# Performance work log

Hardware: AMD Instinct MI355X
Metric: run time of the kernel (lower is better)

Reference implementation:

```python
import jax, jax.numpy as jnp
import numpy as np

B, T, V, D = 8, 256, 32, 256


def setup_inputs() -> dict:
    key = jax.random.key(0)
    k1, k2 = jax.random.split(key)
    # scale by 0.1 so exp(q.k) stays well within fp32 range (dot std ~ 0.1^2*sqrt(D))
    feature = jax.random.normal(k1, (B, T, V, D), dtype=jnp.float32) * 0.1
    feature_aug = jax.random.normal(k2, (B, T, V, D), dtype=jnp.float32) * 0.1
    return {"feature": feature, "feature_aug": feature_aug}


def reference(feature, feature_aug):
    # match torch permute(0,2,1,3): [B,T,V,D] -> [B,V,T,D]
    f = jnp.transpose(feature, (0, 2, 1, 3))      # [B,V,Tq,D]
    fa = jnp.transpose(feature_aug, (0, 2, 1, 3))  # [B,V,Tk,D]
    # all-pairs QK^T scores: [B_i, B_j, V, Tq, Tk]
    scores = jnp.einsum('ivqd,jvkd->ijvqk', f, fa)
    E = jnp.exp(scores)
    # positive (j == i): ap = exp(scores[i,i]).sum over V, Tq -> [B, Tk]
    diag = jnp.einsum('iivqk->ivqk', E)           # [B,V,Tq,Tk]
    ap_exp = diag.sum(axis=(1, 2))                # [B, Tk]
    # negatives (j != i): sum over j,V,Tk minus the j==i part -> [B, Tq]
    total = E.sum(axis=(1, 2, 4))                 # [B, Tq]
    self_part = diag.sum(axis=(1, 3))             # [B, Tq]
    an_exp = total - self_part                    # [B, Tq]
    # per-anchor loss vector [T]; original sums over anchors then takes .mean()
    loss_vec = -jnp.log(ap_exp / an_exp)          # [B, T]
    return loss_vec.sum(axis=0).mean()
```

## Files before the change

kernel.cpp:

```cpp
#include <hip/hip_runtime.h>
#include <hip/hip_bf16.h>


typedef __attribute__((ext_vector_type(4))) float f32x4;
typedef __attribute__((ext_vector_type(2))) long long i64x2;
typedef __attribute__((ext_vector_type(8))) __bf16 bf16x8;
typedef long long i64;

#if __has_builtin(__builtin_amdgcn_exp2f)
#define EXP2(x) __builtin_amdgcn_exp2f(x)
#else
#define EXP2(x) exp2f(x)
#endif

__device__ __forceinline__ unsigned short f2bf(float f) {
    unsigned u = __builtin_bit_cast(unsigned, f);
    u += 0x7FFFu + ((u >> 16) & 1u);
    return (unsigned short)(u >> 16);
}

template <bool HI>
__device__ __forceinline__ unsigned cvt2fp8(float a, float b, unsigned old) {
    return __builtin_amdgcn_cvt_pk_fp8_f32(a, b, old, HI);
}
__device__ __forceinline__ unsigned pack4fp8(float x, float y, float z, float w) {
    return cvt2fp8<true>(z, w, cvt2fp8<false>(x, y, 0u));
}

__device__ __forceinline__ void async16(const void* g, void* l) {
    __builtin_amdgcn_global_load_lds(
        (const __attribute__((address_space(1))) unsigned int*)g,
        (__attribute__((address_space(3))) unsigned int*)l,
        16, 0, 0);
}

template <int CTRL>
__device__ __forceinline__ float dpp_add(float x) {
    int y = __builtin_amdgcn_update_dpp(0, __builtin_bit_cast(int, x),
                                        CTRL, 0xf, 0xf, true);
    return x + __builtin_bit_cast(float, y);
}
__device__ __forceinline__ float rowsum16(float x) {
    x = dpp_add<0x111>(x);
    x = dpp_add<0x112>(x);
    x = dpp_add<0x114>(x);
    x = dpp_add<0x118>(x);
    return x;
}

__global__ __launch_bounds__(256) void infonce_repack_fp8(
    const float* __restrict__ feat, const float* __restrict__ feat_aug,
    unsigned char* __restrict__ pA, unsigned char* __restrict__ pB,
    float* __restrict__ counters)
{
    const int row = blockIdx.x;
    const int tid = threadIdx.x;
    if (blockIdx.x == 0 && blockIdx.y == 0) {
        #pragma unroll
        for (int k = 0; k < 24; ++k) counters[k * 256 + tid] = 0.f;
    }
    const bool isA = (blockIdx.y == 0);
    const float sc = isA ? 1.4426950408889634f : 1.0f;
    const float* src = (isA ? feat : feat_aug) + (size_t)row * 8192;
    unsigned char* dst = (isA ? pA : pB) + (size_t)row * 8192;
    #pragma unroll
    for (int it = 0; it < 2; ++it) {
        const int ob = it * 4096 + tid * 16;
        const int v = ob >> 8;
        const int s = (ob >> 6) & 3;
        const int g = (ob >> 4) & 3;
        const int f1 = v * 256 + s * 64 + g * 8;
        const int f2 = f1 + 32;
        const float4 a0 = *(const float4*)(src + f1);
        const float4 a1 = *(const float4*)(src + f1 + 4);
        const float4 b0 = *(const float4*)(src + f2);
        const float4 b1 = *(const float4*)(src + f2 + 4);
        uint4 p;
        p.x = pack4fp8(a0.x*sc, a0.y*sc, a0.z*sc, a0.w*sc);
        p.y = pack4fp8(a1.x*sc, a1.y*sc, a1.z*sc, a1.w*sc);
        p.z = pack4fp8(b0.x*sc, b0.y*sc, b0.z*sc, b0.w*sc);
        p.w = pack4fp8(b1.x*sc, b1.y*sc, b1.z*sc, b1.w*sc);
        *(uint4*)(dst + ob) = p;
    }
}

__global__ __launch_bounds__(256) void infonce_main_fp8(
    const unsigned char* __restrict__ pA, const unsigned char* __restrict__ pB,
    float* __restrict__ total, float* __restrict__ selfp, float* __restrict__ ap)
{
    __shared__ __align__(16) unsigned char As[2][8192];
    __shared__ __align__(16) unsigned char Bs[2][8192];
    __shared__ float ls_row2[2][128];
    __shared__ float ls_col2[2][128];

    const int tid  = threadIdx.x;
    const int lane = tid & 63;
    const int w    = tid >> 6;
    const int wm   = w >> 1;
    const int wn   = w & 1;
    const int lrow = lane & 15;
    const int quad = lane >> 4;

    const int tileM = blockIdx.x & 15;
    const int tileN = blockIdx.x >> 4;
    const int v     = blockIdx.y;
    const bool diag = (tileM >> 1) == (tileN >> 1);

    const int rl  = w * 32 + (lane >> 2);
    const int cgg = (lane & 3) ^ ((lane >> 3) & 3);
    const unsigned char* aG = pA + ((size_t)(tileM*128 + rl) * 32 + v) * 256 + cgg * 16;
    const unsigned char* bG = pB + ((size_t)(tileN*128 + rl) * 32 + v) * 256 + cgg * 16;

    f32x4 acc[4][4];
    #pragma unroll
    for (int i = 0; i < 4; ++i)
        #pragma unroll
        for (int j = 0; j < 4; ++j)
            acc[i][j] = (f32x4){0.f, 0.f, 0.f, 0.f};

    #pragma unroll
    for (int i = 0; i < 2; ++i) {
        async16(aG + (size_t)i * 16 * 8192, &As[0][w * 2048 + i * 1024]);
        async16(bG + (size_t)i * 16 * 8192, &Bs[0][w * 2048 + i * 1024]);
    }
    __syncthreads();

    const int cgp = (quad ^ ((lrow >> 1) & 3)) * 16;

    #pragma unroll
    for (int s = 0; s < 4; ++s) {
        const int b = s & 1;
        if (s < 3) {
            const int nb = b ^ 1;
            #pragma unroll
            for (int i = 0; i < 2; ++i) {
                async16(aG + (size_t)i * 16 * 8192 + (s + 1) * 64,
                        &As[nb][w * 2048 + i * 1024]);
                async16(bG + (size_t)i * 16 * 8192 + (s + 1) * 64,
                        &Bs[nb][w * 2048 + i * 1024]);
            }
        }
        i64x2 a4[4], b4[4];
        #pragma unroll
        for (int t = 0; t < 4; ++t) {
            a4[t] = *(const i64x2*)&As[b][(wm * 64 + t * 16 + lrow) * 64 + cgp];
            b4[t] = *(const i64x2*)&Bs[b][(wn * 64 + t * 16 + lrow) * 64 + cgp];
        }
        #pragma unroll
        for (int kh = 0; kh < 2; ++kh)
            #pragma unroll
            for (int ti = 0; ti < 4; ++ti)
                #pragma unroll
                for (int tj = 0; tj < 4; ++tj)
                    acc[ti][tj] = __builtin_amdgcn_mfma_f32_16x16x32_fp8_fp8(
                        a4[ti][kh], b4[tj][kh], acc[ti][tj], 0, 0, 0);
        __syncthreads();
    }

    float colp[4] = {0.f, 0.f, 0.f, 0.f};
    #pragma unroll
    for (int ti = 0; ti < 4; ++ti) {
        #pragma unroll
        for (int r = 0; r < 4; ++r) {
            float e0 = EXP2(acc[ti][0][r]);
            float e1 = EXP2(acc[ti][1][r]);
            float e2 = EXP2(acc[ti][2][r]);
            float e3 = EXP2(acc[ti][3][r]);
            if (diag) { colp[0] += e0; colp[1] += e1; colp[2] += e2; colp[3] += e3; }
            float rp = rowsum16((e0 + e1) + (e2 + e3));
            if (lrow == 15)
                ls_row2[wn][wm * 64 + ti * 16 + quad * 4 + r] = rp;
        }
    }
    if (diag) {
        #pragma unroll
        for (int tj = 0; tj < 4; ++tj) {
            float q = colp[tj];
            q += __shfl_xor(q, 16);
            q += __shfl_xor(q, 32);
            if (lane < 16)
                ls_col2[wm][wn * 64 + tj * 16 + lane] = q;
        }
    }
    __syncthreads();
    if (tid < 128) {
        const float rs = ls_row2[0][tid] + ls_row2[1][tid];
        const int rowg = tileM * 128 + tid;
        atomicAdd(&total[rowg], rs);
        if (diag) atomicAdd(&selfp[rowg], rs);
    } else if (diag) {
        const int t2 = tid - 128;
        atomicAdd(&ap[tileN * 128 + t2], ls_col2[0][t2] + ls_col2[1][t2]);
    }
}

__global__ __launch_bounds__(256) void infonce_main_slow(
    const float* __restrict__ feat, const float* __restrict__ feat_aug,
    float* __restrict__ total, float* __restrict__ selfp, float* __restrict__ ap)
{
    __shared__ __align__(16) unsigned short As[128][72];
    __shared__ __align__(16) unsigned short Bs[128][72];
    __shared__ float ls_row[128];
    __shared__ float ls_col[128];

    const int tid  = threadIdx.x;
    const int lane = tid & 63;
    const int w    = tid >> 6;
    const int wm   = w >> 1;
    const int wn   = w & 1;
    const int lrow = lane & 15;
    const int quad = lane >> 4;

    const int tileM = blockIdx.x & 15;
    const int tileN = blockIdx.x >> 4;
    const int v     = blockIdx.y;
    const bool diag = (tileM >> 1) == (tileN >> 1);

    if (tid < 128) ls_row[tid] = 0.0f;
    else           ls_col[tid - 128] = 0.0f;

    const float* aBase = feat     + (size_t)v * 256;
    const float* bBase = feat_aug + (size_t)v * 256;

    f32x4 acc[4][4];
    #pragma unroll
    for (int i = 0; i < 4; ++i)
        #pragma unroll
        for (int j = 0; j < 4; ++j)
            acc[i][j] = (f32x4){0.f, 0.f, 0.f, 0.f};

    const int srow = tid >> 4;
    const int scol = (tid & 15) * 4;

    for (int s = 0; s < 4; ++s) {
        const int k0 = s * 64;
        if (s) __syncthreads();
        #pragma unroll
        for (int it = 0; it < 8; ++it) {
            const int row = it * 16 + srow;
            const float4 a4 = *(const float4*)(aBase + (size_t)(tileM * 128 + row) * 8192 + k0 + scol);
            const float4 b4 = *(const float4*)(bBase + (size_t)(tileN * 128 + row) * 8192 + k0 + scol);
            uint2 wa, wb;
            wa.x = (unsigned)f2bf(a4.x) | ((unsigned)f2bf(a4.y) << 16);
            wa.y = (unsigned)f2bf(a4.z) | ((unsigned)f2bf(a4.w) << 16);
            wb.x = (unsigned)f2bf(b4.x) | ((unsigned)f2bf(b4.y) << 16);
            wb.y = (unsigned)f2bf(b4.z) | ((unsigned)f2bf(b4.w) << 16);
            *(uint2*)&As[row][scol] = wa;
            *(uint2*)&Bs[row][scol] = wb;
        }
        __syncthreads();
        #pragma unroll
        for (int kk = 0; kk < 64; kk += 32) {
            bf16x8 af[4], bfr[4];
            #pragma unroll
            for (int t = 0; t < 4; ++t) {
                af[t]  = *(const bf16x8*)&As[wm * 64 + t * 16 + lrow][kk + quad * 8];
                bfr[t] = *(const bf16x8*)&Bs[wn * 64 + t * 16 + lrow][kk + quad * 8];
            }
            #pragma unroll
            for (int ti = 0; ti < 4; ++ti)
                #pragma unroll
                for (int tj = 0; tj < 4; ++tj)
                    acc[ti][tj] = __builtin_amdgcn_mfma_f32_16x16x32_bf16(
                        af[ti], bfr[tj], acc[ti][tj], 0, 0, 0);
        }
    }

    float colp[4] = {0.f, 0.f, 0.f, 0.f};
    #pragma unroll
    for (int ti = 0; ti < 4; ++ti) {
        #pragma unroll
        for (int r = 0; r < 4; ++r) {
            float e0 = __expf(acc[ti][0][r]);
            float e1 = __expf(acc[ti][1][r]);
            float e2 = __expf(acc[ti][2][r]);
            float e3 = __expf(acc[ti][3][r]);
            colp[0] += e0; colp[1] += e1; colp[2] += e2; colp[3] += e3;
            float rp = (e0 + e1) + (e2 + e3);
            rp += __shfl_xor(rp, 1);
            rp += __shfl_xor(rp, 2);
            rp += __shfl_xor(rp, 4);
            rp += __shfl_xor(rp, 8);
            if (lrow == 0)
                atomicAdd(&ls_row[wm * 64 + ti * 16 + quad * 4 + r], rp);
        }
    }
    if (diag) {
        #pragma unroll
        for (int tj = 0; tj < 4; ++tj) {
            float q = colp[tj];
            q += __shfl_xor(q, 16);
            q += __shfl_xor(q, 32);
            if (lane < 16)
                atomicAdd(&ls_col[wn * 64 + tj * 16 + lane], q);
        }
    }
    __syncthreads();
    if (tid < 128) {
        const float rs = ls_row[tid];
        const int rowg = tileM * 128 + tid;
        atomicAdd(&total[rowg], rs);
        if (diag) atomicAdd(&selfp[rowg], rs);
    } else if (diag) {
        const int t2 = tid - 128;
        atomicAdd(&ap[tileN * 128 + t2], ls_col[t2]);
    }
}

__global__ __launch_bounds__(256) void infonce_finalize(
    const float* __restrict__ total, const float* __restrict__ selfp,
    const float* __restrict__ ap, float* __restrict__ out)
{
    __shared__ float red[4];
    const int tid = threadIdx.x;
    float s = 0.f;
    for (int e = tid; e < 2048; e += 256) {
        const float an = total[e] - selfp[e];
        s += logf(an / ap[e]);
    }
    #pragma unroll
    for (int m = 32; m >= 1; m >>= 1) s += __shfl_xor(s, m);
    if ((tid & 63) == 0) red[tid >> 6] = s;
    __syncthreads();
    if (tid == 0) out[0] = (red[0] + red[1] + red[2] + red[3]) * (1.0f / 256.0f);
}

extern "C" void kernel_launch(void* const* d_in, const int* in_sizes, int n_in,
                              void* d_out, int out_size, void* d_ws, size_t ws_size,
                              hipStream_t stream) {
    const float* feat     = (const float*)d_in[0];
    const float* feat_aug = (const float*)d_in[1];
    float* total = (float*)d_ws;
    float* selfp = total + 2048;
    float* ap    = selfp + 2048;

    const size_t packBytes = (size_t)2048 * 8192;
    const size_t need = 32768 + 2 * packBytes;
    if (ws_size >= need) {
        unsigned char* pA = (unsigned char*)d_ws + 32768;
        unsigned char* pB = pA + packBytes;
        infonce_repack_fp8<<<dim3(2048, 2), 256, 0, stream>>>(feat, feat_aug, pA, pB, total);
        infonce_main_fp8<<<dim3(256, 32), 256, 0, stream>>>(pA, pB, total, selfp, ap);
    } else {
        (void)hipMemsetAsync(d_ws, 0, 3 * 2048 * sizeof(float), stream);
        infonce_main_slow<<<dim3(256, 32), 256, 0, stream>>>(feat, feat_aug, total, selfp, ap);
    }
    infonce_finalize<<<1, 256, 0, stream>>>(total, selfp, ap, (float*)d_out);
}
```

Measured before the change: 207.6 us.

## Switch main GEMM to scaled 16x16x128 MFMA with full-K LDS tile

Replaces the 16x16x32 fp8 MFMA chain with the gfx950 scaled mfma_scale_f32_16x16x128_f8f6f4 (unit scales), cutting the number of MFMA issues per tile by four. The whole K=256 slice for A and B is now loaded into LDS in one shot with an XOR swizzle, instead of a 4-stage double-buffered pipeline, and the repack kernel becomes a plain contiguous conversion. The row/col partial buffers alias the A tile in LDS. The larger 64KB LDS footprint with launch_bounds(256,2) may limit occupancy, and the load/compute overlap from the old pipeline is gone.

```diff
diff --git a/kernel.cpp b/kernel.cpp
--- a/kernel.cpp
+++ b/kernel.cpp
@@ -3,9 +3,9 @@
 
 
 typedef __attribute__((ext_vector_type(4))) float f32x4;
-typedef __attribute__((ext_vector_type(2))) long long i64x2;
+typedef __attribute__((ext_vector_type(4))) int   i32x4;
+typedef __attribute__((ext_vector_type(8))) int   i32x8;
 typedef __attribute__((ext_vector_type(8))) __bf16 bf16x8;
-typedef long long i64;
 
 #if __has_builtin(__builtin_amdgcn_exp2f)
 #define EXP2(x) __builtin_amdgcn_exp2f(x)
@@ -32,6 +32,13 @@
         (const __attribute__((address_space(1))) unsigned int*)g,
         (__attribute__((address_space(3))) unsigned int*)l,
         16, 0, 0);
+}
+
+__device__ __forceinline__ i32x8 cat8(i32x4 lo, i32x4 hi) {
+    i32x8 r;
+    r[0] = lo[0]; r[1] = lo[1]; r[2] = lo[2]; r[3] = lo[3];
+    r[4] = hi[0]; r[5] = hi[1]; r[6] = hi[2]; r[7] = hi[3];
+    return r;
 }
 
 template <int CTRL>
@@ -65,33 +72,28 @@
     unsigned char* dst = (isA ? pA : pB) + (size_t)row * 8192;
     #pragma unroll
     for (int it = 0; it < 2; ++it) {
-        const int ob = it * 4096 + tid * 16;
-        const int v = ob >> 8;
-        const int s = (ob >> 6) & 3;
-        const int g = (ob >> 4) & 3;
-        const int f1 = v * 256 + s * 64 + g * 8;
-        const int f2 = f1 + 32;
-        const float4 a0 = *(const float4*)(src + f1);
-        const float4 a1 = *(const float4*)(src + f1 + 4);
-        const float4 b0 = *(const float4*)(src + f2);
-        const float4 b1 = *(const float4*)(src + f2 + 4);
+        const int base = it * 4096 + tid * 16;
+        const float4 f0 = *(const float4*)(src + base);
+        const float4 f1 = *(const float4*)(src + base + 4);
+        const float4 f2 = *(const float4*)(src + base + 8);
+        const float4 f3 = *(const float4*)(src + base + 12);
         uint4 p;
-        p.x = pack4fp8(a0.x*sc, a0.y*sc, a0.z*sc, a0.w*sc);
-        p.y = pack4fp8(a1.x*sc, a1.y*sc, a1.z*sc, a1.w*sc);
-        p.z = pack4fp8(b0.x*sc, b0.y*sc, b0.z*sc, b0.w*sc);
-        p.w = pack4fp8(b1.x*sc, b1.y*sc, b1.z*sc, b1.w*sc);
-        *(uint4*)(dst + ob) = p;
-    }
-}
-
-__global__ __launch_bounds__(256) void infonce_main_fp8(
+        p.x = pack4fp8(f0.x*sc, f0.y*sc, f0.z*sc, f0.w*sc);
+        p.y = pack4fp8(f1.x*sc, f1.y*sc, f1.z*sc, f1.w*sc);
+        p.z = pack4fp8(f2.x*sc, f2.y*sc, f2.z*sc, f2.w*sc);
+        p.w = pack4fp8(f3.x*sc, f3.y*sc, f3.z*sc, f3.w*sc);
+        *(uint4*)(dst + base) = p;
+    }
+}
+
+__global__ __launch_bounds__(256, 2) void infonce_main_mx(
     const unsigned char* __restrict__ pA, const unsigned char* __restrict__ pB,
     float* __restrict__ total, float* __restrict__ selfp, float* __restrict__ ap)
 {
-    __shared__ __align__(16) unsigned char As[2][8192];
-    __shared__ __align__(16) unsigned char Bs[2][8192];
-    __shared__ float ls_row2[2][128];
-    __shared__ float ls_col2[2][128];
+    __shared__ __align__(16) unsigned char As[128 * 256];
+    __shared__ __align__(16) unsigned char Bs[128 * 256];
+    float (*ls_row2)[128] = (float (*)[128])(void*)As;
+    float (*ls_col2)[128] = (float (*)[128])(void*)(As + 1024);
 
     const int tid  = threadIdx.x;
     const int lane = tid & 63;
@@ -106,10 +108,15 @@
     const int v     = blockIdx.y;
     const bool diag = (tileM >> 1) == (tileN >> 1);
 
-    const int rl  = w * 32 + (lane >> 2);
-    const int cgg = (lane & 3) ^ ((lane >> 3) & 3);
-    const unsigned char* aG = pA + ((size_t)(tileM*128 + rl) * 32 + v) * 256 + cgg * 16;
-    const unsigned char* bG = pB + ((size_t)(tileN*128 + rl) * 32 + v) * 256 + cgg * 16;
+    const size_t vOff = (size_t)v * 256;
+    const size_t rowM = (size_t)(tileM * 128 + w * 32 + quad) * 8192 + vOff;
+    const size_t rowN = (size_t)(tileN * 128 + w * 32 + quad) * 8192 + vOff;
+    #pragma unroll
+    for (int i = 0; i < 8; ++i) {
+        const int lg = (lrow ^ ((i * 4 + quad) & 15)) << 4;
+        async16(pA + rowM + (size_t)i * 4 * 8192 + lg, &As[(w * 32 + i * 4) * 256]);
+        async16(pB + rowN + (size_t)i * 4 * 8192 + lg, &Bs[(w * 32 + i * 4) * 256]);
+    }
 
     f32x4 acc[4][4];
     #pragma unroll
@@ -118,44 +125,32 @@
         for (int j = 0; j < 4; ++j)
             acc[i][j] = (f32x4){0.f, 0.f, 0.f, 0.f};
 
-    #pragma unroll
-    for (int i = 0; i < 2; ++i) {
-        async16(aG + (size_t)i * 16 * 8192, &As[0][w * 2048 + i * 1024]);
-        async16(bG + (size_t)i * 16 * 8192, &Bs[0][w * 2048 + i * 1024]);
-    }
-    __syncthreads();
-
-    const int cgp = (quad ^ ((lrow >> 1) & 3)) * 16;
-
-    #pragma unroll
-    for (int s = 0; s < 4; ++s) {
-        const int b = s & 1;
-        if (s < 3) {
-            const int nb = b ^ 1;
+    __syncthreads();
+
+    #pragma unroll
+    for (int h = 0; h < 2; ++h) {
+        const int g0 = ((h * 8 + quad * 2) ^ lrow) * 16;
+        const int g1 = g0 ^ 16;
+        i32x8 af[4], bf[4];
+        #pragma unroll
+        for (int t = 0; t < 4; ++t) {
+            const int rA = (wm * 64 + t * 16 + lrow) * 256;
+            const int rB = (wn * 64 + t * 16 + lrow) * 256;
+            af[t] = cat8(*(const i32x4*)&As[rA + g0], *(const i32x4*)&As[rA + g1]);
+            bf[t] = cat8(*(const i32x4*)&Bs[rB + g0], *(const i32x4*)&Bs[rB + g1]);
+        }
+        #pragma unroll
+        for (int ti = 0; ti < 4; ++ti)
             #pragma unroll
-            for (int i = 0; i < 2; ++i) {
-                async16(aG + (size_t)i * 16 * 8192 + (s + 1) * 64,
-                        &As[nb][w * 2048 + i * 1024]);
-                async16(bG + (size_t)i * 16 * 8192 + (s + 1) * 64,
-                        &Bs[nb][w * 2048 + i * 1024]);
-            }
-        }
-        i64x2 a4[4], b4[4];
-        #pragma unroll
-        for (int t = 0; t < 4; ++t) {
-            a4[t] = *(const i64x2*)&As[b][(wm * 64 + t * 16 + lrow) * 64 + cgp];
-            b4[t] = *(const i64x2*)&Bs[b][(wn * 64 + t * 16 + lrow) * 64 + cgp];
-        }
-        #pragma unroll
-        for (int kh = 0; kh < 2; ++kh)
-            #pragma unroll
-            for (int ti = 0; ti < 4; ++ti)
-                #pragma unroll
-                for (int tj = 0; tj < 4; ++tj)
-                    acc[ti][tj] = __builtin_amdgcn_mfma_f32_16x16x32_fp8_fp8(
-                        a4[ti][kh], b4[tj][kh], acc[ti][tj], 0, 0, 0);
-        __syncthreads();
-    }
+            for (int tj = 0; tj < 4; ++tj)
+                acc[ti][tj] = __builtin_amdgcn_mfma_scale_f32_16x16x128_f8f6f4(
+                    af[ti], bf[tj], acc[ti][tj],
+                    0, 0,
+                    0, 127,
+                    0, 127);
+    }
+
+    __syncthreads();
 
     float colp[4] = {0.f, 0.f, 0.f, 0.f};
     #pragma unroll
@@ -340,7 +335,7 @@
         unsigned char* pA = (unsigned char*)d_ws + 32768;
         unsigned char* pB = pA + packBytes;
         infonce_repack_fp8<<<dim3(2048, 2), 256, 0, stream>>>(feat, feat_aug, pA, pB, total);
-        infonce_main_fp8<<<dim3(256, 32), 256, 0, stream>>>(pA, pB, total, selfp, ap);
+        infonce_main_mx<<<dim3(256, 32), 256, 0, stream>>>(pA, pB, total, selfp, ap);
     } else {
         (void)hipMemsetAsync(d_ws, 0, 3 * 2048 * sizeof(float), stream);
         infonce_main_slow<<<dim3(256, 32), 256, 0, stream>>>(feat, feat_aug, total, selfp, ap);
```

Measured after the change: 200.1 us. 3.6% less time.
